# Optimization experiments

Measured on AMD Instinct MI355X. Metric: run time of the kernel, lower is better.

Reference implementation:

```python
import jax, jax.numpy as jnp
import numpy as np

MIN_NORM = 1e-15
BALL_EPS = 1e-5  # projection margin for the Poincare ball


def _tanh(x):
    return jnp.tanh(jnp.clip(x, -15.0, 15.0))


def _artanh(x):
    return jnp.arctanh(jnp.clip(x, -1.0 + 1e-5, 1.0 - 1e-5))


def givens_rotations(r, x):
    # r, x: (N, d) with d even -> (N, d)
    g = r.reshape(r.shape[0], -1, 2)
    g = g / jnp.maximum(jnp.linalg.norm(g, axis=-1, keepdims=True), MIN_NORM)
    xp = x.reshape(x.shape[0], -1, 2)
    swap = jnp.concatenate([-xp[..., 1:], xp[..., :1]], axis=-1)
    return (g[..., :1] * xp + g[..., 1:] * swap).reshape(r.shape[0], -1)


def givens_reflection(r, x):
    g = r.reshape(r.shape[0], -1, 2)
    g = g / jnp.maximum(jnp.linalg.norm(g, axis=-1, keepdims=True), MIN_NORM)
    xp = x.reshape(x.shape[0], -1, 2)
    a = jnp.concatenate([xp[..., :1], -xp[..., 1:]], axis=-1)
    b = jnp.concatenate([xp[..., 1:], xp[..., :1]], axis=-1)
    return (g[..., :1] * a + g[..., 1:] * b).reshape(r.shape[0], -1)


def expmap0(u, c):
    sqrt_c = jnp.sqrt(c)
    u_norm = jnp.maximum(jnp.linalg.norm(u, axis=-1, keepdims=True), MIN_NORM)
    return _tanh(sqrt_c * u_norm) * u / (sqrt_c * u_norm)


def mobius_add(x, y, c):
    x2 = jnp.sum(x * x, -1, keepdims=True)
    y2 = jnp.sum(y * y, -1, keepdims=True)
    xy = jnp.sum(x * y, -1, keepdims=True)
    num = (1 + 2 * c * xy + c * y2) * x + (1 - c * x2) * y
    denom = 1 + 2 * c * xy + c * c * x2 * y2
    return num / jnp.maximum(denom, MIN_NORM)


def project(x, c):
    norm = jnp.maximum(jnp.linalg.norm(x, axis=-1, keepdims=True), MIN_NORM)
    maxnorm = (1.0 - BALL_EPS) / jnp.sqrt(c)
    return jnp.where(norm > maxnorm, x / norm * maxnorm, x)


def hyp_distance_multi_c_bmm(x, v, c):
    # x: (nc, cs, d) queries; v: (nc, ns, d) candidates; c: (nc, cs, 1) curvatures
    sqrt_c = jnp.sqrt(c)                                              # (nc, cs, 1)
    vnorm = jnp.linalg.norm(v, axis=-1, keepdims=True).transpose(0, 2, 1)  # (nc, 1, ns)
    xv = jnp.einsum('bcd,bnd->bcn', x, v) / vnorm                     # (nc, cs, ns)
    gamma = _tanh(sqrt_c * vnorm) / sqrt_c                            # (nc, cs, ns)
    x2 = jnp.sum(x * x, -1, keepdims=True)                            # (nc, cs, 1)
    c1 = 1 - 2 * c * gamma * xv + c * gamma ** 2
    c2 = 1 - c * x2
    num = jnp.sqrt(jnp.maximum(c1 ** 2 * x2 + c2 ** 2 * gamma ** 2 - 2 * c1 * c2 * gamma * xv, 0.0))
    denom = 1 - 2 * c * gamma * xv + c ** 2 * gamma ** 2 * x2
    dist = _artanh(sqrt_c * num / jnp.maximum(denom, MIN_NORM))
    return 2 * dist / sqrt_c                                          # (nc, cs, ns)


def setup_inputs() -> dict:
    key = jax.random.key(0)
    nc, cs, ns, d = 16, 1024, 1024, 512
    B = nc * cs
    ks = jax.random.split(key, 8)
    return {
        'head': jax.random.normal(ks[0], (B, d), jnp.float32),
        'head_bias': jax.random.normal(ks[1], (B, 1), jnp.float32),
        'rel': jax.random.normal(ks[2], (B, d), jnp.float32),
        'rel_diag': jax.random.normal(ks[3], (B, 2 * d), jnp.float32),
        'curvature': jax.random.normal(ks[4], (B, 1), jnp.float32),
        'context': jax.random.normal(ks[5], (B, d), jnp.float32),
        'scale': jnp.full((1,), 1.0 / np.sqrt(d), jnp.float32),
        'tail': jax.random.normal(ks[6], (nc * ns, d), jnp.float32),
        'tail_bias': jax.random.normal(ks[7], (nc * ns, 1), jnp.float32),
        'chunk_size': cs,
        'neg_sample_size': ns,
    }


def reference(head, head_bias, rel, rel_diag, curvature, context, scale, tail,
              tail_bias, chunk_size, neg_sample_size):
    num_chunk = head.shape[0] // chunk_size
    d = head.shape[-1]
    c = jax.nn.softplus(curvature)                                    # (B, 1)
    rot_mat, ref_mat = jnp.split(rel_diag, 2, axis=-1)
    rot_q = givens_rotations(rot_mat, head)[:, None, :]               # (B, 1, d)
    ref_q = givens_reflection(ref_mat, head)[:, None, :]              # (B, 1, d)
    cands = jnp.concatenate([ref_q, rot_q], axis=1)                   # (B, 2, d)
    att_w = jax.nn.softmax(
        jnp.sum(context[:, None, :] * cands * scale, -1, keepdims=True), axis=1)
    att_q = jnp.sum(att_w * cands, axis=1)                            # (B, d)
    lhs = expmap0(att_q, c)
    rel_h = expmap0(rel, c)
    res = project(mobius_add(lhs, rel_h, c), c)                       # (B, d)
    x = res.reshape(num_chunk, chunk_size, d)
    v = tail.reshape(num_chunk, neg_sample_size, d)
    c3 = c.reshape(num_chunk, chunk_size, 1)
    dist = hyp_distance_multi_c_bmm(x, v, c3)                         # (nc, cs, ns)
    score = (-dist ** 2
             + head_bias.reshape(num_chunk, chunk_size, 1)
             + tail_bias.reshape(num_chunk, 1, neg_sample_size))
    return score
```

## Files before the change

### kernel.cpp

```cpp
#include <hip/hip_runtime.h>
#include <math.h>

#define DEV static __device__ __forceinline__

constexpr float MIN_NORM = 1e-15f;
constexpr float BALL_EPS = 1e-5f;
constexpr int D = 512;

typedef float f32x4 __attribute__((ext_vector_type(4)));
typedef short short8v __attribute__((ext_vector_type(8)));
typedef unsigned short ushort8v __attribute__((ext_vector_type(8)));

DEV float wave_sum(float v) {
#pragma unroll
    for (int o = 32; o > 0; o >>= 1) v += __shfl_xor(v, o, 64);
    return v;
}

DEV float tanh_clip(float x) {
    x = fminf(fmaxf(x, -15.0f), 15.0f);
    return tanhf(x);
}

DEV unsigned short f2bf(float f) {
    unsigned int u = __float_as_uint(f);
    u = (u + 0x7FFFu + ((u >> 16) & 1u)) >> 16;
    return (unsigned short)u;
}
DEV float bf2f(unsigned short h) { return __uint_as_float(((unsigned int)h) << 16); }

DEV void write_packed_row(unsigned short* pack, size_t nrow, int row,
                          int lane, ushort8v hi, ushort8v lo)
{
    const int kb  = lane >> 2;
    const int cch = lane & 3;
    const int rx  = row & 7;
    unsigned short* dst = pack + ((size_t)kb * nrow + row) * 64;
    *(ushort8v*)(dst + ((cch ^ rx) * 8))       = hi;
    *(ushort8v*)(dst + (((cch + 4) ^ rx) * 8)) = lo;
}

__global__ __launch_bounds__(64)
void preprocess_kernel(const float* __restrict__ head,
                       const float* __restrict__ rel,
                       const float* __restrict__ rel_diag,
                       const float* __restrict__ curvature,
                       const float* __restrict__ context,
                       const float* __restrict__ scale_p,
                       unsigned short* __restrict__ packA,
                       float* __restrict__ row_x2,
                       float* __restrict__ row_c,
                       float* __restrict__ row_sc,
                       int nrow)
{
    const int row  = blockIdx.x;
    const int lane = threadIdx.x;
    const int base = lane * 8;
    const size_t roff = (size_t)row * D;
    const size_t doff = (size_t)row * 2 * D;

    float hv[8], rv[8], gv[8], fv[8], cxv[8];
    *(float4*)&hv[0]  = *(const float4*)(head + roff + base);
    *(float4*)&hv[4]  = *(const float4*)(head + roff + base + 4);
    *(float4*)&rv[0]  = *(const float4*)(rel + roff + base);
    *(float4*)&rv[4]  = *(const float4*)(rel + roff + base + 4);
    *(float4*)&gv[0]  = *(const float4*)(rel_diag + doff + base);
    *(float4*)&gv[4]  = *(const float4*)(rel_diag + doff + base + 4);
    *(float4*)&fv[0]  = *(const float4*)(rel_diag + doff + D + base);
    *(float4*)&fv[4]  = *(const float4*)(rel_diag + doff + D + base + 4);
    *(float4*)&cxv[0] = *(const float4*)(context + roff + base);
    *(float4*)&cxv[4] = *(const float4*)(context + roff + base + 4);

    float rq[8], rf[8];
#pragma unroll
    for (int p = 0; p < 4; ++p) {
        const float x0 = hv[2*p], x1 = hv[2*p+1];
        float g0 = gv[2*p], g1 = gv[2*p+1];
        const float gn = fmaxf(sqrtf(g0*g0 + g1*g1), MIN_NORM);
        g0 /= gn; g1 /= gn;
        rq[2*p]   = g0*x0 - g1*x1;
        rq[2*p+1] = g0*x1 + g1*x0;
        float f0 = fv[2*p], f1 = fv[2*p+1];
        const float fn = fmaxf(sqrtf(f0*f0 + f1*f1), MIN_NORM);
        f0 /= fn; f1 /= fn;
        rf[2*p]   = f0*x0 + f1*x1;
        rf[2*p+1] = f1*x0 - f0*x1;
    }

    float s0=0,s1=0,s2=0,s3=0,s4=0,s5=0,s6=0,s7=0;
#pragma unroll
    for (int e = 0; e < 8; ++e) {
        s0 += cxv[e]*rf[e];   s1 += cxv[e]*rq[e];
        s2 += rv[e]*rv[e];    s3 += rf[e]*rv[e];
        s4 += rq[e]*rv[e];    s5 += rf[e]*rf[e];
        s6 += rq[e]*rq[e];    s7 += rf[e]*rq[e];
    }
    s0 = wave_sum(s0); s1 = wave_sum(s1); s2 = wave_sum(s2); s3 = wave_sum(s3);
    s4 = wave_sum(s4); s5 = wave_sum(s5); s6 = wave_sum(s6); s7 = wave_sum(s7);

    const float cu = curvature[row];
    const float c  = fmaxf(cu, 0.0f) + log1pf(expf(-fabsf(cu)));
    const float sqc = sqrtf(c);
    const float sc  = scale_p[0];

    const float a0 = s0 * sc, a1 = s1 * sc;
    const float mx = fmaxf(a0, a1);
    const float e0 = expf(a0 - mx), e1 = expf(a1 - mx);
    const float w0 = e0 / (e0 + e1);
    const float w1 = 1.0f - w0;

    const float att2    = fmaxf(w0*w0*s5 + 2.0f*w0*w1*s7 + w1*w1*s6, 0.0f);
    const float attdrel = w0*s3 + w1*s4;
    const float u_att = fmaxf(sqrtf(att2), MIN_NORM);
    const float u_rel = fmaxf(sqrtf(s2), MIN_NORM);

    const float kl = tanh_clip(sqc * u_att) / (sqc * u_att);
    const float kr = tanh_clip(sqc * u_rel) / (sqc * u_rel);

    const float x2 = kl*kl*att2;
    const float y2 = kr*kr*s2;
    const float xy = kl*kr*attdrel;

    const float Am  = 1.0f + 2.0f*c*xy + c*y2;
    const float Bm  = 1.0f - c*x2;
    const float den = fmaxf(1.0f + 2.0f*c*xy + c*c*x2*y2, MIN_NORM);
    const float inv_den = 1.0f / den;

    float pre[8];
    float r2p = 0.0f;
#pragma unroll
    for (int e = 0; e < 8; ++e) {
        const float attq = w0*rf[e] + w1*rq[e];
        pre[e] = (Am*kl*attq + Bm*kr*rv[e]) * inv_den;
        r2p += pre[e]*pre[e];
    }
    r2p = wave_sum(r2p);

    const float nrm  = fmaxf(sqrtf(r2p), MIN_NORM);
    const float maxn = (1.0f - BALL_EPS) / sqc;
    const float psc  = (nrm > maxn) ? (maxn / nrm) : 1.0f;

    ushort8v hi, lo;
#pragma unroll
    for (int e = 0; e < 8; ++e) {
        const float o = pre[e] * psc;
        const unsigned short hb_ = f2bf(o);
        hi[e] = hb_;
        lo[e] = f2bf(o - bf2f(hb_));
    }
    write_packed_row(packA, (size_t)nrow, row, lane, hi, lo);

    if (lane == 0) {
        row_x2[row] = r2p * psc * psc;
        row_c[row]  = c;
        row_sc[row] = sqc;
    }
}

__global__ __launch_bounds__(64)
void tailprep_kernel(const float* __restrict__ tail,
                     unsigned short* __restrict__ packB,
                     float* __restrict__ vnorm,
                     int nrow)
{
    const int row  = blockIdx.x;
    const int lane = threadIdx.x;
    const size_t roff = (size_t)row * D + lane * 8;
    float v[8];
    *(float4*)&v[0] = *(const float4*)(tail + roff);
    *(float4*)&v[4] = *(const float4*)(tail + roff + 4);
    float s = 0.0f;
    ushort8v hi, lo;
#pragma unroll
    for (int e = 0; e < 8; ++e) {
        s += v[e]*v[e];
        const unsigned short hb_ = f2bf(v[e]);
        hi[e] = hb_;
        lo[e] = f2bf(v[e] - bf2f(hb_));
    }
    s = wave_sum(s);
    write_packed_row(packB, (size_t)nrow, row, lane, hi, lo);
    if (lane == 0) vnorm[row] = sqrtf(s);
}

__global__ __launch_bounds__(512, 2)
void score_kernel(const unsigned short* __restrict__ packA,
                  const unsigned short* __restrict__ packB,
                  const float* __restrict__ vnorm,
                  const float* __restrict__ row_x2,
                  const float* __restrict__ row_c,
                  const float* __restrict__ row_sc,
                  const float* __restrict__ head_bias,
                  const float* __restrict__ tail_bias,
                  float* __restrict__ out,
                  int cs, int ns, int nrowA, int nrowB)
{
    extern __shared__ __align__(16) char smem[];

    const int orig = blockIdx.x;
    const int wg = (orig & 7) * 32 + (orig >> 3);
    const int bz = wg >> 4;
    const int by = (wg >> 2) & 3;
    const int bx = wg & 3;
    const int m0 = by * 256;
    const int n0 = bx * 256;

    const int tid  = threadIdx.x;
    const int lane = tid & 63;
    const int w    = tid >> 6;
    const int wr   = w >> 2, wn = w & 3;
    const int lrow = lane & 15, lg = lane >> 4;

    f32x4 acc[8][4];
#pragma unroll
    for (int i = 0; i < 8; ++i)
#pragma unroll
        for (int j = 0; j < 4; ++j) acc[i][j] = f32x4{0.f, 0.f, 0.f, 0.f};

    const char* srcA0 = (const char*)packA + (size_t)(bz * cs + m0) * 128;
    const char* srcB0 = (const char*)packB + (size_t)(bz * ns + n0) * 128;
    const size_t strideA = (size_t)nrowA * 128;
    const size_t strideB = (size_t)nrowB * 128;

#define STAGE_HALF(dst, src, half)                                                 \
    do {                                                                           \
        const int bo_ = (half) * 16384 + tid * 16;                                 \
        __builtin_amdgcn_global_load_lds(                                          \
            (const __attribute__((address_space(1))) unsigned int*)((src) + bo_),  \
            (__attribute__((address_space(3))) unsigned int*)((dst) + bo_),        \
            16, 0, 0);                                                             \
        __builtin_amdgcn_global_load_lds(                                          \
            (const __attribute__((address_space(1))) unsigned int*)((src) + bo_ + 8192), \
            (__attribute__((address_space(3))) unsigned int*)((dst) + bo_ + 8192), \
            16, 0, 0);                                                             \
    } while (0)

#define READ_A(M, AH_, AL_)                                                        \
    do {                                                                           \
        const int r_ = wr * 128 + (M) * 16 + lrow;                                 \
        const char* rp_ = curb + r_ * 128;                                         \
        AH_ = *(const short8v*)(rp_ + ((lg    ) ^ (r_ & 7)) * 16);                 \
        AL_ = *(const short8v*)(rp_ + ((lg + 4) ^ (r_ & 7)) * 16);                 \
    } while (0)

#define MFMA_(A_, B_, C_) __builtin_amdgcn_mfma_f32_16x16x32_bf16(A_, B_, C_, 0, 0, 0)

#define TRIPROD(M0, M1)                                                            \
    do {                                                                           \
        _Pragma("unroll") for (int n = 0; n < 4; ++n) acc[M0][n] = MFMA_(ah0, bh[n], acc[M0][n]); \
        _Pragma("unroll") for (int n = 0; n < 4; ++n) acc[M1][n] = MFMA_(ah1, bh[n], acc[M1][n]); \
        _Pragma("unroll") for (int n = 0; n < 4; ++n) acc[M0][n] = MFMA_(ah0, bl[n], acc[M0][n]); \
        _Pragma("unroll") for (int n = 0; n < 4; ++n) acc[M1][n] = MFMA_(ah1, bl[n], acc[M1][n]); \
        _Pragma("unroll") for (int n = 0; n < 4; ++n) acc[M0][n] = MFMA_(al0, bh[n], acc[M0][n]); \
        _Pragma("unroll") for (int n = 0; n < 4; ++n) acc[M1][n] = MFMA_(al1, bh[n], acc[M1][n]); \
    } while (0)

    STAGE_HALF(smem,         srcA0, 0);
    STAGE_HALF(smem,         srcA0, 1);
    STAGE_HALF(smem + 32768, srcB0, 0);
    STAGE_HALF(smem + 32768, srcB0, 1);
    __syncthreads();

#pragma unroll 1
    for (int t = 0; t < 16; ++t) {
        char* curb = smem + (t & 1) * 65536;
        char* nxtb = smem + ((t + 1) & 1) * 65536;
        const char* srcA_n = srcA0 + (size_t)(t + 1) * strideA;
        const char* srcB_n = srcB0 + (size_t)(t + 1) * strideB;
        const bool more = (t < 15);

        short8v bh[4], bl[4];
        short8v ah0, al0, ah1, al1;

        if (more) STAGE_HALF(nxtb + 32768, srcB_n, 0);
#pragma unroll
        for (int n = 0; n < 4; ++n) {
            const int r_ = wn * 64 + n * 16 + lrow;
            const char* rp_ = curb + 32768 + r_ * 128;
            bh[n] = *(const short8v*)(rp_ + ((lg    ) ^ (r_ & 7)) * 16);
            bl[n] = *(const short8v*)(rp_ + ((lg + 4) ^ (r_ & 7)) * 16);
        }
        READ_A(0, ah0, al0);
        READ_A(1, ah1, al1);
        __builtin_amdgcn_s_barrier();
        __builtin_amdgcn_s_setprio(1);
        TRIPROD(0, 1);
        __builtin_amdgcn_s_setprio(0);
        __builtin_amdgcn_s_barrier();

        if (more) STAGE_HALF(nxtb + 32768, srcB_n, 1);
        READ_A(2, ah0, al0);
        READ_A(3, ah1, al1);
        __builtin_amdgcn_s_barrier();
        __builtin_amdgcn_s_setprio(1);
        TRIPROD(2, 3);
        __builtin_amdgcn_s_setprio(0);
        __builtin_amdgcn_s_barrier();

        if (more) STAGE_HALF(nxtb, srcA_n, 0);
        READ_A(4, ah0, al0);
        READ_A(5, ah1, al1);
        __builtin_amdgcn_s_barrier();
        __builtin_amdgcn_s_setprio(1);
        TRIPROD(4, 5);
        __builtin_amdgcn_s_setprio(0);
        __builtin_amdgcn_s_barrier();

        if (more) STAGE_HALF(nxtb, srcA_n, 1);
        READ_A(6, ah0, al0);
        READ_A(7, ah1, al1);
        __builtin_amdgcn_s_barrier();
        __builtin_amdgcn_s_setprio(1);
        TRIPROD(6, 7);
        __builtin_amdgcn_s_setprio(0);

        __syncthreads();
    }

    const int nbase = n0 + wn * 64 + lrow;
    float rvn[4], vnv[4], tb[4];
#pragma unroll
    for (int j = 0; j < 4; ++j) {
        const int gn = bz * ns + nbase + j * 16;
        const float vn = vnorm[gn];
        vnv[j] = vn;
        rvn[j] = 1.0f / vn;
        tb[j]  = tail_bias[gn];
    }
#pragma unroll
    for (int i = 0; i < 8; ++i) {
#pragma unroll
        for (int q = 0; q < 4; ++q) {
            const int gm = bz * cs + m0 + wr * 128 + i * 16 + lg * 4 + q;
            const float x2  = row_x2[gm];
            const float cc  = row_c[gm];
            const float scq = row_sc[gm];
            const float hb  = head_bias[gm];
            const float rscq = 1.0f / scq;
            float* orow = out + (size_t)gm * ns + nbase;
#pragma unroll
            for (int j = 0; j < 4; ++j) {
                const float xv = acc[i][j][q] * rvn[j];
                float xx = fminf(scq * vnv[j], 15.0f);
                const float ey = __expf(2.0f * xx);
                const float g  = (1.0f - 2.0f / (ey + 1.0f)) * rscq;
                const float c1 = 1.0f - 2.0f*cc*g*xv + cc*g*g;
                const float c2 = 1.0f - cc*x2;
                const float num = sqrtf(fmaxf(c1*c1*x2 + c2*c2*g*g - 2.0f*c1*c2*g*xv, 0.0f));
                const float den = fmaxf(1.0f - 2.0f*cc*g*xv + cc*cc*g*g*x2, MIN_NORM);
                float t = scq * num * __builtin_amdgcn_rcpf(den);
                t = fminf(t, 1.0f - 1e-5f);
                const float ath = 0.5f * __logf((1.0f + t) * __builtin_amdgcn_rcpf(1.0f - t));
                const float dist = 2.0f * rscq * ath;
                orow[j * 16] = -dist * dist + hb + tb[j];
            }
        }
    }
#undef STAGE_HALF
#undef READ_A
#undef MFMA_
#undef TRIPROD
}

extern "C" void kernel_launch(void* const* d_in, const int* in_sizes, int n_in,
                              void* d_out, int out_size, void* d_ws, size_t ws_size,
                              hipStream_t stream)
{
    const float* head      = (const float*)d_in[0];
    const float* head_bias = (const float*)d_in[1];
    const float* rel       = (const float*)d_in[2];
    const float* rel_diag  = (const float*)d_in[3];
    const float* curvature = (const float*)d_in[4];
    const float* context   = (const float*)d_in[5];
    const float* scale     = (const float*)d_in[6];
    const float* tail      = (const float*)d_in[7];
    const float* tail_bias = (const float*)d_in[8];

    const int B  = in_sizes[1];
    const int T  = in_sizes[8];
    const int ns = out_size / B;
    const int nc = T / ns;
    const int cs = B / nc;

    unsigned short* packA = (unsigned short*)d_ws;
    unsigned short* packB = packA + (size_t)16 * B * 64;
    float* row_x2 = (float*)(packB + (size_t)16 * T * 64);
    float* row_c  = row_x2 + B;
    float* row_sc = row_c + B;
    float* vnormb = row_sc + B;

    preprocess_kernel<<<B, 64, 0, stream>>>(head, rel, rel_diag, curvature, context,
                                            scale, packA, row_x2, row_c, row_sc, B);
    tailprep_kernel<<<T, 64, 0, stream>>>(tail, packB, vnormb, T);

    (void)hipFuncSetAttribute((const void*)score_kernel,
                              hipFuncAttributeMaxDynamicSharedMemorySize, 131072);
    const int nblk = (ns / 256) * (cs / 256) * nc;
    score_kernel<<<nblk, 512, 131072, stream>>>(packA, packB, vnormb, row_x2, row_c,
                                                row_sc, head_bias, tail_bias,
                                                (float*)d_out, cs, ns, B, T);
}
```

Measured before the change: 136.8 us.

## Merge prep kernels and deepen score GEMM prefetch with quadrant MFMA schedule

Fuses the head and tail preprocessing kernels into one launch, with blocks past B handling tail rows, which saves a kernel launch and the gap between launches. Rewrites the score kernel main loop so global-to-LDS loads run about two K-steps ahead, using partial s_waitcnt vmcnt instead of a full syncthreads. Each step is split into four 4x2 MFMA quadrants that interleave fragment reads with staging. This exposes more memory latency hiding but depends on exact vmcnt counting and buffer reuse ordering, which is fragile.

```diff
diff --git a/kernel.cpp b/kernel.cpp
--- a/kernel.cpp
+++ b/kernel.cpp
@@ -41,21 +41,46 @@
 }
 
 __global__ __launch_bounds__(64)
-void preprocess_kernel(const float* __restrict__ head,
-                       const float* __restrict__ rel,
-                       const float* __restrict__ rel_diag,
-                       const float* __restrict__ curvature,
-                       const float* __restrict__ context,
-                       const float* __restrict__ scale_p,
-                       unsigned short* __restrict__ packA,
-                       float* __restrict__ row_x2,
-                       float* __restrict__ row_c,
-                       float* __restrict__ row_sc,
-                       int nrow)
+void prep_kernel(const float* __restrict__ head,
+                 const float* __restrict__ rel,
+                 const float* __restrict__ rel_diag,
+                 const float* __restrict__ curvature,
+                 const float* __restrict__ context,
+                 const float* __restrict__ scale_p,
+                 const float* __restrict__ tail,
+                 unsigned short* __restrict__ packA,
+                 unsigned short* __restrict__ packB,
+                 float* __restrict__ row_x2,
+                 float* __restrict__ row_c,
+                 float* __restrict__ row_sc,
+                 float* __restrict__ vnorm,
+                 int B, int T)
 {
-    const int row  = blockIdx.x;
     const int lane = threadIdx.x;
     const int base = lane * 8;
+
+    if ((int)blockIdx.x >= B) {
+        const int row = blockIdx.x - B;
+        const size_t roff = (size_t)row * D + base;
+        float v[8];
+        *(float4*)&v[0] = *(const float4*)(tail + roff);
+        *(float4*)&v[4] = *(const float4*)(tail + roff + 4);
+        float s = 0.0f;
+        ushort8v hi, lo;
+#pragma unroll
+        for (int e = 0; e < 8; ++e) {
+            s += v[e]*v[e];
+            const unsigned short hb_ = f2bf(v[e]);
+            hi[e] = hb_;
+            lo[e] = f2bf(v[e] - bf2f(hb_));
+        }
+        s = wave_sum(s);
+        write_packed_row(packB, (size_t)T, row, lane, hi, lo);
+        if (lane == 0) vnorm[row] = sqrtf(s);
+        return;
+    }
+
+    const int row = blockIdx.x;
     const size_t roff = (size_t)row * D;
     const size_t doff = (size_t)row * 2 * D;
 
@@ -148,39 +173,13 @@
         hi[e] = hb_;
         lo[e] = f2bf(o - bf2f(hb_));
     }
-    write_packed_row(packA, (size_t)nrow, row, lane, hi, lo);
+    write_packed_row(packA, (size_t)B, row, lane, hi, lo);
 
     if (lane == 0) {
         row_x2[row] = r2p * psc * psc;
         row_c[row]  = c;
         row_sc[row] = sqc;
     }
-}
-
-__global__ __launch_bounds__(64)
-void tailprep_kernel(const float* __restrict__ tail,
-                     unsigned short* __restrict__ packB,
-                     float* __restrict__ vnorm,
-                     int nrow)
-{
-    const int row  = blockIdx.x;
-    const int lane = threadIdx.x;
-    const size_t roff = (size_t)row * D + lane * 8;
-    float v[8];
-    *(float4*)&v[0] = *(const float4*)(tail + roff);
-    *(float4*)&v[4] = *(const float4*)(tail + roff + 4);
-    float s = 0.0f;
-    ushort8v hi, lo;
-#pragma unroll
-    for (int e = 0; e < 8; ++e) {
-        s += v[e]*v[e];
-        const unsigned short hb_ = f2bf(v[e]);
-        hi[e] = hb_;
-        lo[e] = f2bf(v[e] - bf2f(hb_));
-    }
-    s = wave_sum(s);
-    write_packed_row(packB, (size_t)nrow, row, lane, hi, lo);
-    if (lane == 0) vnorm[row] = sqrtf(s);
 }
 
 __global__ __launch_bounds__(512, 2)
@@ -217,104 +216,104 @@
 #pragma unroll
         for (int j = 0; j < 4; ++j) acc[i][j] = f32x4{0.f, 0.f, 0.f, 0.f};
 
-    const char* srcA0 = (const char*)packA + (size_t)(bz * cs + m0) * 128;
-    const char* srcB0 = (const char*)packB + (size_t)(bz * ns + n0) * 128;
-    const size_t strideA = (size_t)nrowA * 128;
-    const size_t strideB = (size_t)nrowB * 128;
-
-#define STAGE_HALF(dst, src, half)                                                 \
-    do {                                                                           \
-        const int bo_ = (half) * 16384 + tid * 16;                                 \
-        __builtin_amdgcn_global_load_lds(                                          \
-            (const __attribute__((address_space(1))) unsigned int*)((src) + bo_),  \
-            (__attribute__((address_space(3))) unsigned int*)((dst) + bo_),        \
-            16, 0, 0);                                                             \
-        __builtin_amdgcn_global_load_lds(                                          \
-            (const __attribute__((address_space(1))) unsigned int*)((src) + bo_ + 8192), \
-            (__attribute__((address_space(3))) unsigned int*)((dst) + bo_ + 8192), \
-            16, 0, 0);                                                             \
+    const int xr = (lg ^ (lrow & 7)) * 16;
+    const int baseA = (wr * 128 + lrow) * 128 + xr;
+    const int baseB = 32768 + (wn * 64 + lrow) * 128 + xr;
+
+    const int s16 = (tid & 255) * 16;
+    const int shi = tid >> 8;
+
+    const char* gA = (const char*)packA + (size_t)(bz * cs + m0) * 128;
+    const char* gB = (const char*)packB + (size_t)(bz * ns + n0) * 128;
+    const size_t strA = (size_t)nrowA * 128;
+    const size_t strB = (size_t)nrowB * 128;
+
+#define GLL(srcp, dstp)                                                        \
+    __builtin_amdgcn_global_load_lds(                                          \
+        (const __attribute__((address_space(1))) unsigned int*)(srcp),         \
+        (__attribute__((address_space(3))) unsigned int*)(dstp), 16, 0, 0)
+
+#define STAGE(dstbase, srcpanel, off0, sstr)                                   \
+    do { const int o_ = (off0) + s16 + shi * (sstr);                           \
+         GLL((srcpanel) + o_, (dstbase) + o_); } while (0)
+
+#define STAGE_A0(d, s) do { STAGE(d, s, 0, 4096);     STAGE(d, s, 16384, 4096); } while (0)
+#define STAGE_A1(d, s) do { STAGE(d, s, 8192, 4096);  STAGE(d, s, 24576, 4096); } while (0)
+#define STAGE_B0(d, s) do { STAGE(d, s, 0, 8192);     STAGE(d, s, 16384, 8192); } while (0)
+#define STAGE_B1(d, s) do { STAGE(d, s, 4096, 8192);  STAGE(d, s, 20480, 8192); } while (0)
+
+#define RD(p, off) (*(const short8v*)((p) + (off)))
+#define MFMA_(A_, B_, C_) __builtin_amdgcn_mfma_f32_16x16x32_bf16(A_, B_, C_, 0, 0, 0)
+
+#define QUAD(MOFF, NOFF)                                                       \
+    do {                                                                       \
+        _Pragma("unroll") for (int mm = 0; mm < 4; ++mm)                       \
+        _Pragma("unroll") for (int nn = 0; nn < 2; ++nn)                       \
+            acc[(MOFF)+mm][(NOFF)+nn] = MFMA_(ah[mm], bh[(NOFF)+nn], acc[(MOFF)+mm][(NOFF)+nn]); \
+        _Pragma("unroll") for (int mm = 0; mm < 4; ++mm)                       \
+        _Pragma("unroll") for (int nn = 0; nn < 2; ++nn)                       \
+            acc[(MOFF)+mm][(NOFF)+nn] = MFMA_(ah[mm], bl[(NOFF)+nn], acc[(MOFF)+mm][(NOFF)+nn]); \
+        _Pragma("unroll") for (int mm = 0; mm < 4; ++mm)                       \
+        _Pragma("unroll") for (int nn = 0; nn < 2; ++nn)                       \
+            acc[(MOFF)+mm][(NOFF)+nn] = MFMA_(al[mm], bh[(NOFF)+nn], acc[(MOFF)+mm][(NOFF)+nn]); \
     } while (0)
 
-#define READ_A(M, AH_, AL_)                                                        \
-    do {                                                                           \
-        const int r_ = wr * 128 + (M) * 16 + lrow;                                 \
-        const char* rp_ = curb + r_ * 128;                                         \
-        AH_ = *(const short8v*)(rp_ + ((lg    ) ^ (r_ & 7)) * 16);                 \
-        AL_ = *(const short8v*)(rp_ + ((lg + 4) ^ (r_ & 7)) * 16);                 \
-    } while (0)
-
-#define MFMA_(A_, B_, C_) __builtin_amdgcn_mfma_f32_16x16x32_bf16(A_, B_, C_, 0, 0, 0)
-
-#define TRIPROD(M0, M1)                                                            \
-    do {                                                                           \
-        _Pragma("unroll") for (int n = 0; n < 4; ++n) acc[M0][n] = MFMA_(ah0, bh[n], acc[M0][n]); \
-        _Pragma("unroll") for (int n = 0; n < 4; ++n) acc[M1][n] = MFMA_(ah1, bh[n], acc[M1][n]); \
-        _Pragma("unroll") for (int n = 0; n < 4; ++n) acc[M0][n] = MFMA_(ah0, bl[n], acc[M0][n]); \
-        _Pragma("unroll") for (int n = 0; n < 4; ++n) acc[M1][n] = MFMA_(ah1, bl[n], acc[M1][n]); \
-        _Pragma("unroll") for (int n = 0; n < 4; ++n) acc[M0][n] = MFMA_(al0, bh[n], acc[M0][n]); \
-        _Pragma("unroll") for (int n = 0; n < 4; ++n) acc[M1][n] = MFMA_(al1, bh[n], acc[M1][n]); \
-    } while (0)
-
-    STAGE_HALF(smem,         srcA0, 0);
-    STAGE_HALF(smem,         srcA0, 1);
-    STAGE_HALF(smem + 32768, srcB0, 0);
-    STAGE_HALF(smem + 32768, srcB0, 1);
-    __syncthreads();
+#define BAR()   __builtin_amdgcn_s_barrier()
+#define PRIO(x) __builtin_amdgcn_s_setprio(x)
+
+    STAGE_A0(smem, gA);               STAGE_A1(smem, gA);
+    STAGE_B0(smem + 32768, gB);       STAGE_B1(smem + 32768, gB);
+    STAGE_A0(smem + 65536, gA + strA);
+    STAGE_B0(smem + 98304, gB + strB);
+    STAGE_B1(smem + 98304, gB + strB);
+    asm volatile("s_waitcnt vmcnt(6)" ::: "memory");
+    BAR();
+
+    short8v ah[4], al[4], bh[4], bl[4];
 
 #pragma unroll 1
     for (int t = 0; t < 16; ++t) {
-        char* curb = smem + (t & 1) * 65536;
-        char* nxtb = smem + ((t + 1) & 1) * 65536;
-        const char* srcA_n = srcA0 + (size_t)(t + 1) * strideA;
-        const char* srcB_n = srcB0 + (size_t)(t + 1) * strideB;
-        const bool more = (t < 15);
-
-        short8v bh[4], bl[4];
-        short8v ah0, al0, ah1, al1;
-
-        if (more) STAGE_HALF(nxtb + 32768, srcB_n, 0);
-#pragma unroll
-        for (int n = 0; n < 4; ++n) {
-            const int r_ = wn * 64 + n * 16 + lrow;
-            const char* rp_ = curb + 32768 + r_ * 128;
-            bh[n] = *(const short8v*)(rp_ + ((lg    ) ^ (r_ & 7)) * 16);
-            bl[n] = *(const short8v*)(rp_ + ((lg + 4) ^ (r_ & 7)) * 16);
-        }
-        READ_A(0, ah0, al0);
-        READ_A(1, ah1, al1);
-        __builtin_amdgcn_s_barrier();
-        __builtin_amdgcn_s_setprio(1);
-        TRIPROD(0, 1);
-        __builtin_amdgcn_s_setprio(0);
-        __builtin_amdgcn_s_barrier();
-
-        if (more) STAGE_HALF(nxtb + 32768, srcB_n, 1);
-        READ_A(2, ah0, al0);
-        READ_A(3, ah1, al1);
-        __builtin_amdgcn_s_barrier();
-        __builtin_amdgcn_s_setprio(1);
-        TRIPROD(2, 3);
-        __builtin_amdgcn_s_setprio(0);
-        __builtin_amdgcn_s_barrier();
-
-        if (more) STAGE_HALF(nxtb, srcA_n, 0);
-        READ_A(4, ah0, al0);
-        READ_A(5, ah1, al1);
-        __builtin_amdgcn_s_barrier();
-        __builtin_amdgcn_s_setprio(1);
-        TRIPROD(4, 5);
-        __builtin_amdgcn_s_setprio(0);
-        __builtin_amdgcn_s_barrier();
-
-        if (more) STAGE_HALF(nxtb, srcA_n, 1);
-        READ_A(6, ah0, al0);
-        READ_A(7, ah1, al1);
-        __builtin_amdgcn_s_barrier();
-        __builtin_amdgcn_s_setprio(1);
-        TRIPROD(6, 7);
-        __builtin_amdgcn_s_setprio(0);
-
-        __syncthreads();
+        char* cur = smem + (t & 1) * 65536;
+        char* oth = smem + ((t + 1) & 1) * 65536;
+        const char* gA1 = gA + (size_t)(t + 1) * strA;
+        const char* gA2 = gA + (size_t)(t + 2) * strA;
+        const char* gB2 = gB + (size_t)(t + 2) * strB;
+
+        if (t < 15) STAGE_A1(oth, gA1);
+#pragma unroll
+        for (int m = 0; m < 4; ++m) {
+            ah[m] = RD(cur, baseA + m * 2048);
+            al[m] = RD(cur, (baseA ^ 64) + m * 2048);
+        }
+#pragma unroll
+        for (int n = 0; n < 2; ++n) {
+            bh[n] = RD(cur, baseB + n * 2048);
+            bl[n] = RD(cur, (baseB ^ 64) + n * 2048);
+        }
+        BAR(); PRIO(1); QUAD(0, 0); PRIO(0); BAR();
+
+        if (t < 14) STAGE_A0(cur, gA2);
+#pragma unroll
+        for (int n = 2; n < 4; ++n) {
+            bh[n] = RD(cur, baseB + n * 2048);
+            bl[n] = RD(cur, (baseB ^ 64) + n * 2048);
+        }
+        BAR(); PRIO(1); QUAD(0, 2); PRIO(0); BAR();
+
+        if (t < 14) STAGE_B0(cur + 32768, gB2);
+#pragma unroll
+        for (int m = 0; m < 4; ++m) {
+            ah[m] = RD(cur, baseA + 8192 + m * 2048);
+            al[m] = RD(cur, (baseA ^ 64) + 8192 + m * 2048);
+        }
+        BAR(); PRIO(1); QUAD(4, 2); PRIO(0); BAR();
+
+        if (t < 14) STAGE_B1(cur + 32768, gB2);
+        BAR(); PRIO(1); QUAD(4, 0); PRIO(0);
+
+        if (t <= 13)      asm volatile("s_waitcnt vmcnt(6)" ::: "memory");
+        else if (t == 14) asm volatile("s_waitcnt vmcnt(0)" ::: "memory");
+        BAR();
     }
 
     const int nbase = n0 + wn * 64 + lrow;
@@ -348,18 +347,25 @@
                 const float c2 = 1.0f - cc*x2;
                 const float num = sqrtf(fmaxf(c1*c1*x2 + c2*c2*g*g - 2.0f*c1*c2*g*xv, 0.0f));
                 const float den = fmaxf(1.0f - 2.0f*cc*g*xv + cc*cc*g*g*x2, MIN_NORM);
-                float t = scq * num * __builtin_amdgcn_rcpf(den);
-                t = fminf(t, 1.0f - 1e-5f);
-                const float ath = 0.5f * __logf((1.0f + t) * __builtin_amdgcn_rcpf(1.0f - t));
+                float tt = scq * num * __builtin_amdgcn_rcpf(den);
+                tt = fminf(tt, 1.0f - 1e-5f);
+                const float ath = 0.5f * __logf((1.0f + tt) * __builtin_amdgcn_rcpf(1.0f - tt));
                 const float dist = 2.0f * rscq * ath;
                 orow[j * 16] = -dist * dist + hb + tb[j];
             }
         }
     }
-#undef STAGE_HALF
-#undef READ_A
+#undef GLL
+#undef STAGE
+#undef STAGE_A0
+#undef STAGE_A1
+#undef STAGE_B0
+#undef STAGE_B1
+#undef RD
 #undef MFMA_
-#undef TRIPROD
+#undef QUAD
+#undef BAR
+#undef PRIO
 }
 
 extern "C" void kernel_launch(void* const* d_in, const int* in_sizes, int n_in,
@@ -389,9 +395,9 @@
     float* row_sc = row_c + B;
     float* vnormb = row_sc + B;
 
-    preprocess_kernel<<<B, 64, 0, stream>>>(head, rel, rel_diag, curvature, context,
-                                            scale, packA, row_x2, row_c, row_sc, B);
-    tailprep_kernel<<<T, 64, 0, stream>>>(tail, packB, vnormb, T);
+    prep_kernel<<<B + T, 64, 0, stream>>>(head, rel, rel_diag, curvature, context,
+                                          scale, tail, packA, packB,
+                                          row_x2, row_c, row_sc, vnormb, B, T);
 
     (void)hipFuncSetAttribute((const void*)score_kernel,
                               hipFuncAttributeMaxDynamicSharedMemorySize, 131072);
```

Result: no change. 135.1 us (-1.2%).
